# Kernel optimization log

Hardware: AMD Instinct MI355X
Metric: run time of the kernel (lower is better)

Reference implementation:

```python
import jax, jax.numpy as jnp
import numpy as np

LOSS_WEIGHT = 1.0
RADIUS = 1
DILATION = 2

def _mind_shift_indices():
    # six-neighbourhood offsets in a 3x3x3 kernel (as in torch code)
    six = np.array([[0, 1, 1], [1, 1, 0], [1, 0, 1], [1, 1, 2], [2, 1, 1], [1, 2, 1]])
    dist = ((six[:, None, :] - six[None, :, :]) ** 2).sum(-1)
    x, y = np.meshgrid(np.arange(6), np.arange(6), indexing='ij')
    mask = ((x > y) & (dist == 2)).reshape(-1)
    idx1 = np.repeat(six, 6, axis=0)[mask]
    idx2 = np.tile(six, (6, 1))[mask]
    return idx1, idx2

_IDX1, _IDX2 = _mind_shift_indices()

def _shifted(padded, idx, d, D, H, W):
    # one-hot dilated conv == static slice of replication-padded volume
    outs = [padded[:, :, a * d:a * d + D, b * d:b * d + H, c * d:c * d + W]
            for (a, b, c) in idx]
    return jnp.concatenate(outs, axis=1)  # (N, 12, D, H, W)

def mind_ssc(img, radius=RADIUS, dilation=DILATION):
    N, C, D, H, W = img.shape
    p = dilation
    padded = jnp.pad(img, ((0, 0), (0, 0), (p, p), (p, p), (p, p)), mode='edge')
    diff2 = (_shifted(padded, _IDX1, dilation, D, H, W)
             - _shifted(padded, _IDX2, dilation, D, H, W)) ** 2
    r = radius
    k = 2 * r + 1
    diff2p = jnp.pad(diff2, ((0, 0), (0, 0), (r, r), (r, r), (r, r)), mode='edge')
    ssd = jax.lax.reduce_window(diff2p, 0.0, jax.lax.add,
                                (1, 1, k, k, k), (1, 1, 1, 1, 1), 'VALID') / (k ** 3)
    mind = ssd - jnp.min(ssd, axis=1, keepdims=True)
    mind_var = jnp.mean(mind, axis=1, keepdims=True)
    m = jax.lax.stop_gradient(jnp.mean(mind_var))  # torch uses .item() -> detached
    mind_var = jnp.clip(mind_var, m * 0.001, m * 1000.0)
    return jnp.exp(-mind / mind_var)

def setup_inputs() -> dict:
    key = jax.random.key(0)
    k1, k2 = jax.random.split(key)
    shape = (2, 1, 128, 128, 128)
    predict = jax.random.normal(k1, shape, dtype=jnp.float32)
    target = jax.random.normal(k2, shape, dtype=jnp.float32)
    return {"predict": predict, "target": target}

def reference(predict, target):
    loss = jnp.mean((mind_ssc(predict) - mind_ssc(target)) ** 2)
    return loss * LOSS_WEIGHT
```

## Files before the change

### kernel.cpp

```cpp
#include <hip/hip_runtime.h>


#define DIM 128
#define HW (128 * 128)
#define DHW (128 * 128 * 128)
#define NVOX (2 * DHW)
#define LOSS_COUNT (2.0 * 12.0 * DHW)

#define TS   16
#define SY   18
#define NSP  (SY * TS)
#define CHZ  16
#define PSTR 7

typedef float f4 __attribute__((ext_vector_type(4)));
typedef float f2 __attribute__((ext_vector_type(2)));

__device__ __forceinline__ int clampi(int v) {
    v = v < 0 ? 0 : v;
    return v > 127 ? 127 : v;
}

__device__ __forceinline__ unsigned fkey(float f) {
    unsigned u = __float_as_uint(f);
    return (u & 0x80000000u) ? ~u : (u | 0x80000000u);
}
__device__ __forceinline__ float fdec(unsigned k) {
    unsigned u = (k & 0x80000000u) ? (k ^ 0x80000000u) : ~k;
    return __uint_as_float(u);
}

__device__ __forceinline__ void block_reduce_atomic(float v, double* dst) {
#pragma unroll
    for (int off = 32; off > 0; off >>= 1)
        v += __shfl_down(v, off, 64);
    __shared__ float red[4];
    int lane = threadIdx.x & 63;
    int wid  = threadIdx.x >> 6;
    if (lane == 0) red[wid] = v;
    __syncthreads();
    if (threadIdx.x == 0) {
        double t = (double)red[0] + (double)red[1] + (double)red[2] + (double)red[3];
        atomicAdd(dst, t);
    }
    __syncthreads();
}

__device__ __forceinline__ void block_minmax_atomic(float mnp, float mxp,
                                                    float mnt, float mxt,
                                                    unsigned* keys) {
#pragma unroll
    for (int off = 32; off > 0; off >>= 1) {
        mnp = fminf(mnp, __shfl_down(mnp, off, 64));
        mxp = fmaxf(mxp, __shfl_down(mxp, off, 64));
        mnt = fminf(mnt, __shfl_down(mnt, off, 64));
        mxt = fmaxf(mxt, __shfl_down(mxt, off, 64));
    }
    __shared__ float r[4][4];
    int lane = threadIdx.x & 63, wid = threadIdx.x >> 6;
    if (lane == 0) { r[wid][0] = mnp; r[wid][1] = mxp; r[wid][2] = mnt; r[wid][3] = mxt; }
    __syncthreads();
    if (threadIdx.x == 0) {
        float a = fminf(fminf(r[0][0], r[1][0]), fminf(r[2][0], r[3][0]));
        float b = fmaxf(fmaxf(r[0][1], r[1][1]), fmaxf(r[2][1], r[3][1]));
        float c = fminf(fminf(r[0][2], r[1][2]), fminf(r[2][2], r[3][2]));
        float d = fmaxf(fmaxf(r[0][3], r[1][3]), fmaxf(r[2][3], r[3][3]));
        atomicMin(&keys[0], fkey(a));
        atomicMax(&keys[1], fkey(b));
        atomicMin(&keys[2], fkey(c));
        atomicMax(&keys[3], fkey(d));
    }
    __syncthreads();
}

struct SPos {
    int y0, ym, yp;
    int cx[3], cm[3], cp[3];
    int woff;
};

__device__ __forceinline__ SPos make_spos(int p, int y0t, int x0t, int stride) {
    SPos q;
    int py = p >> 4, px = p & 15;
    int gy = clampi(y0t - 1 + py);
    int gx = x0t + px;
    q.y0 = gy * DIM; q.ym = clampi(gy - 2) * DIM; q.yp = clampi(gy + 2) * DIM;
#pragma unroll
    for (int wx = 0; wx < 3; ++wx) {
        int c = clampi(gx + wx - 1);
        q.cx[wx] = c;
        q.cm[wx] = clampi(c - 2);
        q.cp[wx] = clampi(c + 2);
    }
    q.woff = p * stride;
    return q;
}


__device__ __forceinline__ void stage_pair(const float* __restrict__ ip,
                                           const float* __restrict__ tp,
                                           int zm, int zc, int zp,
                                           const SPos& q, f4* __restrict__ X) {
    f2 acc[12];
#pragma unroll
    for (int c = 0; c < 12; ++c) acc[c] = (f2)0.0f;
#pragma unroll
    for (int wx = 0; wx < 3; ++wx) {
        int o0 = zm + q.y0 + q.cx[wx];
        int o1 = zc + q.y0 + q.cm[wx];
        int o2 = zc + q.ym + q.cx[wx];
        int o3 = zc + q.y0 + q.cp[wx];
        int o4 = zp + q.y0 + q.cx[wx];
        int o5 = zc + q.yp + q.cx[wx];
        f2 s0 = {ip[o0], tp[o0]};
        f2 s1 = {ip[o1], tp[o1]};
        f2 s2 = {ip[o2], tp[o2]};
        f2 s3 = {ip[o3], tp[o3]};
        f2 s4 = {ip[o4], tp[o4]};
        f2 s5 = {ip[o5], tp[o5]};
        f2 d;
        d = s1 - s0; acc[0]  += d * d;
        d = s2 - s0; acc[1]  += d * d;
        d = s2 - s1; acc[2]  += d * d;
        d = s3 - s0; acc[3]  += d * d;
        d = s3 - s2; acc[4]  += d * d;
        d = s4 - s1; acc[5]  += d * d;
        d = s4 - s2; acc[6]  += d * d;
        d = s4 - s3; acc[7]  += d * d;
        d = s5 - s0; acc[8]  += d * d;
        d = s5 - s1; acc[9]  += d * d;
        d = s5 - s3; acc[10] += d * d;
        d = s5 - s4; acc[11] += d * d;
    }
#pragma unroll
    for (int k = 0; k < 6; ++k) {
        f4 w;
        w.x = acc[2 * k].x;     w.y = acc[2 * k].y;
        w.z = acc[2 * k + 1].x; w.w = acc[2 * k + 1].y;
        X[q.woff + k] = w;
    }
}

__device__ __forceinline__ void box3y_pair(const f4* __restrict__ X,
                                           int ty, int tx, f4 q[6]) {
    int b0 = ((ty + 0) * TS + tx) * PSTR;
    int b1 = ((ty + 1) * TS + tx) * PSTR;
    int b2 = ((ty + 2) * TS + tx) * PSTR;
#pragma unroll
    for (int k = 0; k < 6; ++k)
        q[k] = X[b0 + k] + X[b1 + k] + X[b2 + k];
}

__global__ __launch_bounds__(256, 4) void fused_kernel(const float* __restrict__ pred,
                                                       const float* __restrict__ targ,
                                                       double* __restrict__ acc,
                                                       unsigned* __restrict__ keys) {
    __shared__ f4 X[NSP * PSTR];
    const int t = threadIdx.x;
    const int tile = blockIdx.x & 63, n = blockIdx.x >> 6;
    const int x0t = (tile & 7) * TS, y0t = (tile >> 3) * TS;
    const int z0 = blockIdx.y * CHZ;
    const float* ip = pred + (size_t)n * DHW;
    const float* tp = targ + (size_t)n * DHW;

    SPos pa = make_spos(t, y0t, x0t, PSTR);
    const bool hasB = (t + 256) < NSP;
    SPos pb = make_spos(hasB ? (t + 256) : 0, y0t, x0t, PSTR);

    const int ty = t >> 4, tx = t & 15;

    f4 A[6], B[6];
#pragma unroll
    for (int k = 0; k < 6; ++k) { A[k] = (f4)0.0f; B[k] = (f4)0.0f; }

    float vsump = 0.0f, vsumt = 0.0f, lsum = 0.0f;
    float locmnp = 1e30f, locmxp = -1e30f, locmnt = 1e30f, locmxt = -1e30f;

    for (int tz = z0 - 1; tz <= z0 + CHZ; ++tz) {
        int zq = clampi(tz);
        int zc = zq * HW, zm = clampi(zq - 2) * HW, zp = clampi(zq + 2) * HW;
        stage_pair(ip, tp, zm, zc, zp, pa, X);
        if (hasB) stage_pair(ip, tp, zm, zc, zp, pb, X);
        __syncthreads();

        f4 q[6];
        box3y_pair(X, ty, tx, q);
        __syncthreads();

        int ze = tz - 1;
        if (ze >= z0) {
            f4 v[6];
#pragma unroll
            for (int k = 0; k < 6; ++k) v[k] = A[k] + q[k];

            float mnp = v[0][0], mnt = v[0][1];
            float smp = 0.0f, smt = 0.0f;
#pragma unroll
            for (int c = 0; c < 12; ++c) {
                float pv = v[c >> 1][(c & 1) * 2];
                float tv = v[c >> 1][(c & 1) * 2 + 1];
                mnp = fminf(mnp, pv); smp += pv;
                mnt = fminf(mnt, tv); smt += tv;
            }
            float varp = smp * (1.0f / 12.0f) - mnp;
            float vart = smt * (1.0f / 12.0f) - mnt;
            vsump += varp; vsumt += vart;
            locmnp = fminf(locmnp, varp); locmxp = fmaxf(locmxp, varp);
            locmnt = fminf(locmnt, vart); locmxt = fmaxf(locmxt, vart);

            float invp = -1.0f / varp;
            float invt = -1.0f / vart;
            float la = 0.0f;
#pragma unroll
            for (int c = 0; c < 12; ++c) {
                float pv = v[c >> 1][(c & 1) * 2];
                float tv = v[c >> 1][(c & 1) * 2 + 1];
                float ep = __expf((pv - mnp) * invp);
                float et = __expf((tv - mnt) * invt);
                float dd = ep - et;
                la += dd * dd;
            }
            lsum += la;
        }
#pragma unroll
        for (int k = 0; k < 6; ++k) { A[k] = B[k] + q[k]; B[k] = q[k]; }
    }

    block_reduce_atomic(vsump, &acc[0]);
    block_reduce_atomic(vsumt, &acc[1]);
    block_reduce_atomic(lsum,  &acc[2]);
    block_minmax_atomic(locmnp, locmxp, locmnt, locmxt, keys);
}


__global__ void init_kernel(double* __restrict__ acc, unsigned* __restrict__ keys) {
    acc[0] = 0.0; acc[1] = 0.0; acc[2] = 0.0; acc[3] = 0.0;
    keys[0] = 0xFFFFFFFFu; keys[1] = 0u;
    keys[2] = 0xFFFFFFFFu; keys[3] = 0u;
    keys[4] = 0u;
}

__global__ void flag_kernel(const double* __restrict__ acc, unsigned* __restrict__ keys) {
    float m_p = (float)(acc[0] * (1.0 / (double)NVOX));
    float m_t = (float)(acc[1] * (1.0 / (double)NVOX));
    float mnp = fdec(keys[0]), mxp = fdec(keys[1]);
    float mnt = fdec(keys[2]), mxt = fdec(keys[3]);
    bool clean = (mnp >= m_p * 0.001f) && (mxp <= m_p * 1000.0f) &&
                 (mnt >= m_t * 0.001f) && (mxt <= m_t * 1000.0f);
    keys[4] = clean ? 0u : 1u;
}

__device__ __forceinline__ void stage_xsum(const float* __restrict__ im,
                                           int zm, int zc, int zp,
                                           const SPos& q, f4* __restrict__ P) {
    f4 a = (f4)0.0f, b = (f4)0.0f, c = (f4)0.0f;
#pragma unroll
    for (int wx = 0; wx < 3; ++wx) {
        float s0 = im[zm + q.y0 + q.cx[wx]];
        float s1 = im[zc + q.y0 + q.cm[wx]];
        float s2 = im[zc + q.ym + q.cx[wx]];
        float s3 = im[zc + q.y0 + q.cp[wx]];
        float s4 = im[zp + q.y0 + q.cx[wx]];
        float s5 = im[zc + q.yp + q.cx[wx]];
        float d;
        d = s1 - s0; a.x += d * d;
        d = s2 - s0; a.y += d * d;
        d = s2 - s1; a.z += d * d;
        d = s3 - s0; a.w += d * d;
        d = s3 - s2; b.x += d * d;
        d = s4 - s1; b.y += d * d;
        d = s4 - s2; b.z += d * d;
        d = s4 - s3; b.w += d * d;
        d = s5 - s0; c.x += d * d;
        d = s5 - s1; c.y += d * d;
        d = s5 - s3; c.z += d * d;
        d = s5 - s4; c.w += d * d;
    }
    P[q.woff + 0] = a;
    P[q.woff + 1] = b;
    P[q.woff + 2] = c;
}

__device__ __forceinline__ void box3y(const f4* __restrict__ P,
                                      int ty, int tx, f4 q[3]) {
    int base = (ty * TS + tx) * 3;
#pragma unroll
    for (int k = 0; k < 3; ++k)
        q[k] = P[base + k] + P[base + TS * 3 + k] + P[base + 2 * TS * 3 + k];
}

__device__ __forceinline__ float min12(const f4 v[3]) {
    float mn = v[0][0];
#pragma unroll
    for (int i = 0; i < 4; ++i)
        mn = fminf(mn, fminf(v[0][i], fminf(v[1][i], v[2][i])));
    return mn;
}
__device__ __forceinline__ float sum12(const f4 v[3]) {
    float sm = 0.0f;
#pragma unroll
    for (int i = 0; i < 4; ++i)
        sm += v[0][i] + v[1][i] + v[2][i];
    return sm;
}

__global__ __launch_bounds__(256, 4) void loss_kernel(const float* __restrict__ pred,
                                                      const float* __restrict__ targ,
                                                      const double* __restrict__ acc,
                                                      const unsigned* __restrict__ keys,
                                                      double* __restrict__ loss_sum) {
    if (keys[4] == 0u) return;

    __shared__ f4 Xp[NSP * 3];
    __shared__ f4 Xt[NSP * 3];
    const int t = threadIdx.x;
    const int tile = blockIdx.x & 63, n = blockIdx.x >> 6;
    const int x0t = (tile & 7) * TS, y0t = (tile >> 3) * TS;
    const int z0 = blockIdx.y * CHZ;
    const float* ip = pred + (size_t)n * DHW;
    const float* tp = targ + (size_t)n * DHW;

    const float m_p = (float)(acc[0] * (1.0 / (double)NVOX));
    const float m_t = (float)(acc[1] * (1.0 / (double)NVOX));

    SPos pa = make_spos(t, y0t, x0t, 3);
    const bool hasB = (t + 256) < NSP;
    SPos pb = make_spos(hasB ? (t + 256) : 0, y0t, x0t, 3);

    const int ty = t >> 4, tx = t & 15;

    f4 Ap[3], Bp[3], At[3], Bt[3];
#pragma unroll
    for (int q = 0; q < 3; ++q) {
        Ap[q] = (f4)0.0f; Bp[q] = (f4)0.0f;
        At[q] = (f4)0.0f; Bt[q] = (f4)0.0f;
    }
    float lsum = 0.0f;

    for (int tz = z0 - 1; tz <= z0 + CHZ; ++tz) {
        int zq = clampi(tz);
        int zc = zq * HW, zm = clampi(zq - 2) * HW, zp = clampi(zq + 2) * HW;
        stage_xsum(ip, zm, zc, zp, pa, Xp);
        stage_xsum(tp, zm, zc, zp, pa, Xt);
        if (hasB) {
            stage_xsum(ip, zm, zc, zp, pb, Xp);
            stage_xsum(tp, zm, zc, zp, pb, Xt);
        }
        __syncthreads();

        f4 qp[3], qt[3];
        box3y(Xp, ty, tx, qp);
        box3y(Xt, ty, tx, qt);
        __syncthreads();

        int ze = tz - 1;
        if (ze >= z0) {
            f4 vp[3], vt[3];
#pragma unroll
            for (int q = 0; q < 3; ++q) {
                vp[q] = Ap[q] + qp[q];
                vt[q] = At[q] + qt[q];
            }
            float mnp = min12(vp), smp = sum12(vp);
            float mnt = min12(vt), smt = sum12(vt);
            float varp = smp * (1.0f / 12.0f) - mnp;
            varp = fminf(fmaxf(varp, m_p * 0.001f), m_p * 1000.0f);
            float invp = -1.0f / varp;
            float vart = smt * (1.0f / 12.0f) - mnt;
            vart = fminf(fmaxf(vart, m_t * 0.001f), m_t * 1000.0f);
            float invt = -1.0f / vart;

            float a = 0.0f;
#pragma unroll
            for (int q = 0; q < 3; ++q)
#pragma unroll
                for (int i = 0; i < 4; ++i) {
                    float ep = __expf((vp[q][i] - mnp) * invp);
                    float et = __expf((vt[q][i] - mnt) * invt);
                    float dd = ep - et;
                    a += dd * dd;
                }
            lsum += a;
        }
#pragma unroll
        for (int q = 0; q < 3; ++q) {
            Ap[q] = Bp[q] + qp[q]; Bp[q] = qp[q];
            At[q] = Bt[q] + qt[q]; Bt[q] = qt[q];
        }
    }

    block_reduce_atomic(lsum, loss_sum);
}

__global__ void finalize_kernel(const double* __restrict__ acc,
                                const unsigned* __restrict__ keys,
                                float* __restrict__ out) {
    double l = (keys[4] == 0u) ? acc[2] : acc[3];
    out[0] = (float)(l * (1.0 / LOSS_COUNT));
}

extern "C" void kernel_launch(void* const* d_in, const int* in_sizes, int n_in,
                              void* d_out, int out_size, void* d_ws, size_t ws_size,
                              hipStream_t stream) {
    const float* pred = (const float*)d_in[0];
    const float* targ = (const float*)d_in[1];
    float* out = (float*)d_out;
    double* acc = (double*)d_ws;
    unsigned* keys = (unsigned*)((char*)d_ws + 64);

    dim3 block(256);
    dim3 grid(128, 8);

    init_kernel<<<1, 1, 0, stream>>>(acc, keys);
    fused_kernel<<<grid, block, 0, stream>>>(pred, targ, acc, keys);
    flag_kernel<<<1, 1, 0, stream>>>(acc, keys);
    loss_kernel<<<grid, block, 0, stream>>>(pred, targ, acc, keys, &acc[3]);
    finalize_kernel<<<1, 1, 0, stream>>>(acc, keys, out);
}
```

Measured before the change: 167.0 us.

## Merge five launches into one cooperative kernel with grid syncs

Result: slower. 519.2 us (+210.9%).

```diff
diff --git a/kernel.cpp b/kernel.cpp
--- a/kernel.cpp
+++ b/kernel.cpp
@@ -1,5 +1,8 @@
 #include <hip/hip_runtime.h>
-
+#include <hip/hip_cooperative_groups.h>
+
+
+namespace cg = cooperative_groups;
 
 #define DIM 128
 #define HW (128 * 128)
@@ -96,22 +99,23 @@
     return q;
 }
 
-
 __device__ __forceinline__ void stage_pair(const float* __restrict__ ip,
                                            const float* __restrict__ tp,
                                            int zm, int zc, int zp,
                                            const SPos& q, f4* __restrict__ X) {
+    const int r0 = zm + q.y0, r1 = zc + q.y0, r2 = zc + q.ym;
+    const int r3 = zc + q.yp, r4 = zp + q.y0;
     f2 acc[12];
 #pragma unroll
     for (int c = 0; c < 12; ++c) acc[c] = (f2)0.0f;
 #pragma unroll
     for (int wx = 0; wx < 3; ++wx) {
-        int o0 = zm + q.y0 + q.cx[wx];
-        int o1 = zc + q.y0 + q.cm[wx];
-        int o2 = zc + q.ym + q.cx[wx];
-        int o3 = zc + q.y0 + q.cp[wx];
-        int o4 = zp + q.y0 + q.cx[wx];
-        int o5 = zc + q.yp + q.cx[wx];
+        int o0 = r0 + q.cx[wx];
+        int o1 = r1 + q.cm[wx];
+        int o2 = r2 + q.cx[wx];
+        int o3 = r1 + q.cp[wx];
+        int o4 = r4 + q.cx[wx];
+        int o5 = r3 + q.cx[wx];
         f2 s0 = {ip[o0], tp[o0]};
         f2 s1 = {ip[o1], tp[o1]};
         f2 s2 = {ip[o2], tp[o2]};
@@ -151,117 +155,20 @@
         q[k] = X[b0 + k] + X[b1 + k] + X[b2 + k];
 }
 
-__global__ __launch_bounds__(256, 4) void fused_kernel(const float* __restrict__ pred,
-                                                       const float* __restrict__ targ,
-                                                       double* __restrict__ acc,
-                                                       unsigned* __restrict__ keys) {
-    __shared__ f4 X[NSP * PSTR];
-    const int t = threadIdx.x;
-    const int tile = blockIdx.x & 63, n = blockIdx.x >> 6;
-    const int x0t = (tile & 7) * TS, y0t = (tile >> 3) * TS;
-    const int z0 = blockIdx.y * CHZ;
-    const float* ip = pred + (size_t)n * DHW;
-    const float* tp = targ + (size_t)n * DHW;
-
-    SPos pa = make_spos(t, y0t, x0t, PSTR);
-    const bool hasB = (t + 256) < NSP;
-    SPos pb = make_spos(hasB ? (t + 256) : 0, y0t, x0t, PSTR);
-
-    const int ty = t >> 4, tx = t & 15;
-
-    f4 A[6], B[6];
-#pragma unroll
-    for (int k = 0; k < 6; ++k) { A[k] = (f4)0.0f; B[k] = (f4)0.0f; }
-
-    float vsump = 0.0f, vsumt = 0.0f, lsum = 0.0f;
-    float locmnp = 1e30f, locmxp = -1e30f, locmnt = 1e30f, locmxt = -1e30f;
-
-    for (int tz = z0 - 1; tz <= z0 + CHZ; ++tz) {
-        int zq = clampi(tz);
-        int zc = zq * HW, zm = clampi(zq - 2) * HW, zp = clampi(zq + 2) * HW;
-        stage_pair(ip, tp, zm, zc, zp, pa, X);
-        if (hasB) stage_pair(ip, tp, zm, zc, zp, pb, X);
-        __syncthreads();
-
-        f4 q[6];
-        box3y_pair(X, ty, tx, q);
-        __syncthreads();
-
-        int ze = tz - 1;
-        if (ze >= z0) {
-            f4 v[6];
-#pragma unroll
-            for (int k = 0; k < 6; ++k) v[k] = A[k] + q[k];
-
-            float mnp = v[0][0], mnt = v[0][1];
-            float smp = 0.0f, smt = 0.0f;
-#pragma unroll
-            for (int c = 0; c < 12; ++c) {
-                float pv = v[c >> 1][(c & 1) * 2];
-                float tv = v[c >> 1][(c & 1) * 2 + 1];
-                mnp = fminf(mnp, pv); smp += pv;
-                mnt = fminf(mnt, tv); smt += tv;
-            }
-            float varp = smp * (1.0f / 12.0f) - mnp;
-            float vart = smt * (1.0f / 12.0f) - mnt;
-            vsump += varp; vsumt += vart;
-            locmnp = fminf(locmnp, varp); locmxp = fmaxf(locmxp, varp);
-            locmnt = fminf(locmnt, vart); locmxt = fmaxf(locmxt, vart);
-
-            float invp = -1.0f / varp;
-            float invt = -1.0f / vart;
-            float la = 0.0f;
-#pragma unroll
-            for (int c = 0; c < 12; ++c) {
-                float pv = v[c >> 1][(c & 1) * 2];
-                float tv = v[c >> 1][(c & 1) * 2 + 1];
-                float ep = __expf((pv - mnp) * invp);
-                float et = __expf((tv - mnt) * invt);
-                float dd = ep - et;
-                la += dd * dd;
-            }
-            lsum += la;
-        }
-#pragma unroll
-        for (int k = 0; k < 6; ++k) { A[k] = B[k] + q[k]; B[k] = q[k]; }
-    }
-
-    block_reduce_atomic(vsump, &acc[0]);
-    block_reduce_atomic(vsumt, &acc[1]);
-    block_reduce_atomic(lsum,  &acc[2]);
-    block_minmax_atomic(locmnp, locmxp, locmnt, locmxt, keys);
-}
-
-
-__global__ void init_kernel(double* __restrict__ acc, unsigned* __restrict__ keys) {
-    acc[0] = 0.0; acc[1] = 0.0; acc[2] = 0.0; acc[3] = 0.0;
-    keys[0] = 0xFFFFFFFFu; keys[1] = 0u;
-    keys[2] = 0xFFFFFFFFu; keys[3] = 0u;
-    keys[4] = 0u;
-}
-
-__global__ void flag_kernel(const double* __restrict__ acc, unsigned* __restrict__ keys) {
-    float m_p = (float)(acc[0] * (1.0 / (double)NVOX));
-    float m_t = (float)(acc[1] * (1.0 / (double)NVOX));
-    float mnp = fdec(keys[0]), mxp = fdec(keys[1]);
-    float mnt = fdec(keys[2]), mxt = fdec(keys[3]);
-    bool clean = (mnp >= m_p * 0.001f) && (mxp <= m_p * 1000.0f) &&
-                 (mnt >= m_t * 0.001f) && (mxt <= m_t * 1000.0f);
-    keys[4] = clean ? 0u : 1u;
-}
-
 __device__ __forceinline__ void stage_xsum(const float* __restrict__ im,
                                            int zm, int zc, int zp,
                                            const SPos& q, f4* __restrict__ P) {
+    const int r0 = zm + q.y0, r1 = zc + q.y0, r2 = zc + q.ym;
+    const int r3 = zc + q.yp, r4 = zp + q.y0;
     f4 a = (f4)0.0f, b = (f4)0.0f, c = (f4)0.0f;
 #pragma unroll
     for (int wx = 0; wx < 3; ++wx) {
-        float s0 = im[zm + q.y0 + q.cx[wx]];
-        float s1 = im[zc + q.y0 + q.cm[wx]];
-        float s2 = im[zc + q.ym + q.cx[wx]];
-        float s3 = im[zc + q.y0 + q.cp[wx]];
-        float s4 = im[zp + q.y0 + q.cx[wx]];
-        float s5 = im[zc + q.yp + q.cx[wx]];
+        float s0 = im[r0 + q.cx[wx]];
+        float s1 = im[r1 + q.cm[wx]];
+        float s2 = im[r2 + q.cx[wx]];
+        float s3 = im[r1 + q.cp[wx]];
+        float s4 = im[r4 + q.cx[wx]];
+        float s5 = im[r3 + q.cx[wx]];
         float d;
         d = s1 - s0; a.x += d * d;
         d = s2 - s0; a.y += d * d;
@@ -304,6 +211,293 @@
     return sm;
 }
 
+
+__global__ __launch_bounds__(256, 4) void mono_kernel(const float* __restrict__ pred,
+                                                      const float* __restrict__ targ,
+                                                      double* __restrict__ acc,
+                                                      unsigned* __restrict__ keys,
+                                                      float* __restrict__ out) {
+    cg::grid_group grid = cg::this_grid();
+
+    __shared__ f4 X[NSP * PSTR];
+
+    const int t = threadIdx.x;
+    const int tile = blockIdx.x & 63, n = blockIdx.x >> 6;
+    const int x0t = (tile & 7) * TS, y0t = (tile >> 3) * TS;
+    const int z0 = blockIdx.y * CHZ;
+    const float* ip = pred + (size_t)n * DHW;
+    const float* tp = targ + (size_t)n * DHW;
+    const bool isB0 = (blockIdx.x == 0 && blockIdx.y == 0);
+
+    if (isB0 && t == 0) {
+        acc[0] = 0.0; acc[1] = 0.0; acc[2] = 0.0; acc[3] = 0.0;
+        keys[0] = 0xFFFFFFFFu; keys[1] = 0u;
+        keys[2] = 0xFFFFFFFFu; keys[3] = 0u;
+    }
+    grid.sync();
+
+    SPos pa = make_spos(t, y0t, x0t, PSTR);
+    const bool hasB = (t + 256) < NSP;
+    SPos pb = make_spos(hasB ? (t + 256) : 0, y0t, x0t, PSTR);
+    const int ty = t >> 4, tx = t & 15;
+
+    {
+        f4 A[6], B[6];
+#pragma unroll
+        for (int k = 0; k < 6; ++k) { A[k] = (f4)0.0f; B[k] = (f4)0.0f; }
+
+        float vsump = 0.0f, vsumt = 0.0f, lsum = 0.0f;
+        float locmnp = 1e30f, locmxp = -1e30f, locmnt = 1e30f, locmxt = -1e30f;
+
+        for (int tz = z0 - 1; tz <= z0 + CHZ; ++tz) {
+            int zq = clampi(tz);
+            int zc = zq * HW, zm = clampi(zq - 2) * HW, zp = clampi(zq + 2) * HW;
+            stage_pair(ip, tp, zm, zc, zp, pa, X);
+            if (hasB) stage_pair(ip, tp, zm, zc, zp, pb, X);
+            __syncthreads();
+
+            f4 q[6];
+            box3y_pair(X, ty, tx, q);
+            __syncthreads();
+
+            int ze = tz - 1;
+            if (ze >= z0) {
+                f4 v[6];
+#pragma unroll
+                for (int k = 0; k < 6; ++k) v[k] = A[k] + q[k];
+
+                float mnp = v[0][0], mnt = v[0][1];
+                float smp = 0.0f, smt = 0.0f;
+#pragma unroll
+                for (int c = 0; c < 12; ++c) {
+                    float pv = v[c >> 1][(c & 1) * 2];
+                    float tv = v[c >> 1][(c & 1) * 2 + 1];
+                    mnp = fminf(mnp, pv); smp += pv;
+                    mnt = fminf(mnt, tv); smt += tv;
+                }
+                float varp = smp * (1.0f / 12.0f) - mnp;
+                float vart = smt * (1.0f / 12.0f) - mnt;
+                vsump += varp; vsumt += vart;
+                locmnp = fminf(locmnp, varp); locmxp = fmaxf(locmxp, varp);
+                locmnt = fminf(locmnt, vart); locmxt = fmaxf(locmxt, vart);
+
+                float invp = -1.0f / varp;
+                float invt = -1.0f / vart;
+                float la = 0.0f;
+#pragma unroll
+                for (int c = 0; c < 12; ++c) {
+                    float pv = v[c >> 1][(c & 1) * 2];
+                    float tv = v[c >> 1][(c & 1) * 2 + 1];
+                    float ep = __expf((pv - mnp) * invp);
+                    float et = __expf((tv - mnt) * invt);
+                    float dd = ep - et;
+                    la += dd * dd;
+                }
+                lsum += la;
+            }
+#pragma unroll
+            for (int k = 0; k < 6; ++k) { A[k] = B[k] + q[k]; B[k] = q[k]; }
+        }
+
+        block_reduce_atomic(vsump, &acc[0]);
+        block_reduce_atomic(vsumt, &acc[1]);
+        block_reduce_atomic(lsum,  &acc[2]);
+        block_minmax_atomic(locmnp, locmxp, locmnt, locmxt, keys);
+    }
+    __threadfence();
+    grid.sync();
+
+    __shared__ float s_mp, s_mt;
+    __shared__ int s_clean;
+    if (t == 0) {
+        double a0 = __hip_atomic_load(&acc[0], __ATOMIC_RELAXED, __HIP_MEMORY_SCOPE_AGENT);
+        double a1 = __hip_atomic_load(&acc[1], __ATOMIC_RELAXED, __HIP_MEMORY_SCOPE_AGENT);
+        unsigned k0 = __hip_atomic_load(&keys[0], __ATOMIC_RELAXED, __HIP_MEMORY_SCOPE_AGENT);
+        unsigned k1 = __hip_atomic_load(&keys[1], __ATOMIC_RELAXED, __HIP_MEMORY_SCOPE_AGENT);
+        unsigned k2 = __hip_atomic_load(&keys[2], __ATOMIC_RELAXED, __HIP_MEMORY_SCOPE_AGENT);
+        unsigned k3 = __hip_atomic_load(&keys[3], __ATOMIC_RELAXED, __HIP_MEMORY_SCOPE_AGENT);
+        float m_p = (float)(a0 * (1.0 / (double)NVOX));
+        float m_t = (float)(a1 * (1.0 / (double)NVOX));
+        bool clean = (fdec(k0) >= m_p * 0.001f) && (fdec(k1) <= m_p * 1000.0f) &&
+                     (fdec(k2) >= m_t * 0.001f) && (fdec(k3) <= m_t * 1000.0f);
+        s_mp = m_p; s_mt = m_t; s_clean = clean ? 1 : 0;
+    }
+    __syncthreads();
+    const bool clean = (s_clean != 0);
+    const float m_p = s_mp, m_t = s_mt;
+
+    if (!clean) {
+        f4* Xp = X;
+        f4* Xt = X + NSP * 3;
+        SPos fa = make_spos(t, y0t, x0t, 3);
+        SPos fb = make_spos(hasB ? (t + 256) : 0, y0t, x0t, 3);
+
+        f4 Ap[3], Bp[3], At[3], Bt[3];
+#pragma unroll
+        for (int q = 0; q < 3; ++q) {
+            Ap[q] = (f4)0.0f; Bp[q] = (f4)0.0f;
+            At[q] = (f4)0.0f; Bt[q] = (f4)0.0f;
+        }
+        float lsum = 0.0f;
+
+        for (int tz = z0 - 1; tz <= z0 + CHZ; ++tz) {
+            int zq = clampi(tz);
+            int zc = zq * HW, zm = clampi(zq - 2) * HW, zp = clampi(zq + 2) * HW;
+            stage_xsum(ip, zm, zc, zp, fa, Xp);
+            stage_xsum(tp, zm, zc, zp, fa, Xt);
+            if (hasB) {
+                stage_xsum(ip, zm, zc, zp, fb, Xp);
+                stage_xsum(tp, zm, zc, zp, fb, Xt);
+            }
+            __syncthreads();
+
+            f4 qp[3], qt[3];
+            box3y(Xp, ty, tx, qp);
+            box3y(Xt, ty, tx, qt);
+            __syncthreads();
+
+            int ze = tz - 1;
+            if (ze >= z0) {
+                f4 vp[3], vt[3];
+#pragma unroll
+                for (int q = 0; q < 3; ++q) {
+                    vp[q] = Ap[q] + qp[q];
+                    vt[q] = At[q] + qt[q];
+                }
+                float mnp = min12(vp), smp = sum12(vp);
+                float mnt = min12(vt), smt = sum12(vt);
+                float varp = smp * (1.0f / 12.0f) - mnp;
+                varp = fminf(fmaxf(varp, m_p * 0.001f), m_p * 1000.0f);
+                float invp = -1.0f / varp;
+                float vart = smt * (1.0f / 12.0f) - mnt;
+                vart = fminf(fmaxf(vart, m_t * 0.001f), m_t * 1000.0f);
+                float invt = -1.0f / vart;
+
+                float a = 0.0f;
+#pragma unroll
+                for (int q = 0; q < 3; ++q)
+#pragma unroll
+                    for (int i = 0; i < 4; ++i) {
+                        float ep = __expf((vp[q][i] - mnp) * invp);
+                        float et = __expf((vt[q][i] - mnt) * invt);
+                        float dd = ep - et;
+                        a += dd * dd;
+                    }
+                lsum += a;
+            }
+#pragma unroll
+            for (int q = 0; q < 3; ++q) {
+                Ap[q] = Bp[q] + qp[q]; Bp[q] = qp[q];
+                At[q] = Bt[q] + qt[q]; Bt[q] = qt[q];
+            }
+        }
+        block_reduce_atomic(lsum, &acc[3]);
+        __threadfence();
+    }
+    grid.sync();
+
+    if (isB0 && t == 0) {
+        double l = clean
+            ? __hip_atomic_load(&acc[2], __ATOMIC_RELAXED, __HIP_MEMORY_SCOPE_AGENT)
+            : __hip_atomic_load(&acc[3], __ATOMIC_RELAXED, __HIP_MEMORY_SCOPE_AGENT);
+        out[0] = (float)(l * (1.0 / LOSS_COUNT));
+    }
+}
+
+
+__global__ void init_kernel(double* __restrict__ acc, unsigned* __restrict__ keys) {
+    acc[0] = 0.0; acc[1] = 0.0; acc[2] = 0.0; acc[3] = 0.0;
+    keys[0] = 0xFFFFFFFFu; keys[1] = 0u;
+    keys[2] = 0xFFFFFFFFu; keys[3] = 0u;
+    keys[4] = 0u;
+}
+
+__global__ __launch_bounds__(256, 4) void fused_kernel(const float* __restrict__ pred,
+                                                       const float* __restrict__ targ,
+                                                       double* __restrict__ acc,
+                                                       unsigned* __restrict__ keys) {
+    __shared__ f4 X[NSP * PSTR];
+    const int t = threadIdx.x;
+    const int tile = blockIdx.x & 63, n = blockIdx.x >> 6;
+    const int x0t = (tile & 7) * TS, y0t = (tile >> 3) * TS;
+    const int z0 = blockIdx.y * CHZ;
+    const float* ip = pred + (size_t)n * DHW;
+    const float* tp = targ + (size_t)n * DHW;
+
+    SPos pa = make_spos(t, y0t, x0t, PSTR);
+    const bool hasB = (t + 256) < NSP;
+    SPos pb = make_spos(hasB ? (t + 256) : 0, y0t, x0t, PSTR);
+    const int ty = t >> 4, tx = t & 15;
+
+    f4 A[6], B[6];
+#pragma unroll
+    for (int k = 0; k < 6; ++k) { A[k] = (f4)0.0f; B[k] = (f4)0.0f; }
+
+    float vsump = 0.0f, vsumt = 0.0f, lsum = 0.0f;
+    float locmnp = 1e30f, locmxp = -1e30f, locmnt = 1e30f, locmxt = -1e30f;
+
+    for (int tz = z0 - 1; tz <= z0 + CHZ; ++tz) {
+        int zq = clampi(tz);
+        int zc = zq * HW, zm = clampi(zq - 2) * HW, zp = clampi(zq + 2) * HW;
+        stage_pair(ip, tp, zm, zc, zp, pa, X);
+        if (hasB) stage_pair(ip, tp, zm, zc, zp, pb, X);
+        __syncthreads();
+
+        f4 q[6];
+        box3y_pair(X, ty, tx, q);
+        __syncthreads();
+
+        int ze = tz - 1;
+        if (ze >= z0) {
+            f4 v[6];
+#pragma unroll
+            for (int k = 0; k < 6; ++k) v[k] = A[k] + q[k];
+            float mnp = v[0][0], mnt = v[0][1];
+            float smp = 0.0f, smt = 0.0f;
+#pragma unroll
+            for (int c = 0; c < 12; ++c) {
+                float pv = v[c >> 1][(c & 1) * 2];
+                float tv = v[c >> 1][(c & 1) * 2 + 1];
+                mnp = fminf(mnp, pv); smp += pv;
+                mnt = fminf(mnt, tv); smt += tv;
+            }
+            float varp = smp * (1.0f / 12.0f) - mnp;
+            float vart = smt * (1.0f / 12.0f) - mnt;
+            vsump += varp; vsumt += vart;
+            locmnp = fminf(locmnp, varp); locmxp = fmaxf(locmxp, varp);
+            locmnt = fminf(locmnt, vart); locmxt = fmaxf(locmxt, vart);
+            float invp = -1.0f / varp;
+            float invt = -1.0f / vart;
+            float la = 0.0f;
+#pragma unroll
+            for (int c = 0; c < 12; ++c) {
+                float pv = v[c >> 1][(c & 1) * 2];
+                float tv = v[c >> 1][(c & 1) * 2 + 1];
+                float ep = __expf((pv - mnp) * invp);
+                float et = __expf((tv - mnt) * invt);
+                float dd = ep - et;
+                la += dd * dd;
+            }
+            lsum += la;
+        }
+#pragma unroll
+        for (int k = 0; k < 6; ++k) { A[k] = B[k] + q[k]; B[k] = q[k]; }
+    }
+
+    block_reduce_atomic(vsump, &acc[0]);
+    block_reduce_atomic(vsumt, &acc[1]);
+    block_reduce_atomic(lsum,  &acc[2]);
+    block_minmax_atomic(locmnp, locmxp, locmnt, locmxt, keys);
+}
+
+__global__ void flag_kernel(const double* __restrict__ acc, unsigned* __restrict__ keys) {
+    float m_p = (float)(acc[0] * (1.0 / (double)NVOX));
+    float m_t = (float)(acc[1] * (1.0 / (double)NVOX));
+    bool clean = (fdec(keys[0]) >= m_p * 0.001f) && (fdec(keys[1]) <= m_p * 1000.0f) &&
+                 (fdec(keys[2]) >= m_t * 0.001f) && (fdec(keys[3]) <= m_t * 1000.0f);
+    keys[4] = clean ? 0u : 1u;
+}
+
 __global__ __launch_bounds__(256, 4) void loss_kernel(const float* __restrict__ pred,
                                                       const float* __restrict__ targ,
                                                       const double* __restrict__ acc,
@@ -326,7 +520,6 @@
     SPos pa = make_spos(t, y0t, x0t, 3);
     const bool hasB = (t + 256) < NSP;
     SPos pb = make_spos(hasB ? (t + 256) : 0, y0t, x0t, 3);
-
     const int ty = t >> 4, tx = t & 15;
 
     f4 Ap[3], Bp[3], At[3], Bt[3];
@@ -411,9 +604,14 @@
     dim3 block(256);
     dim3 grid(128, 8);
 
-    init_kernel<<<1, 1, 0, stream>>>(acc, keys);
-    fused_kernel<<<grid, block, 0, stream>>>(pred, targ, acc, keys);
-    flag_kernel<<<1, 1, 0, stream>>>(acc, keys);
-    loss_kernel<<<grid, block, 0, stream>>>(pred, targ, acc, keys, &acc[3]);
-    finalize_kernel<<<1, 1, 0, stream>>>(acc, keys, out);
-}
+    void* args[] = {(void*)&pred, (void*)&targ, (void*)&acc, (void*)&keys, (void*)&out};
+    hipError_t e = hipLaunchCooperativeKernel((void*)mono_kernel, grid, block,
+                                              args, 0, stream);
+    if (e != hipSuccess) {
+        init_kernel<<<1, 1, 0, stream>>>(acc, keys);
+        fused_kernel<<<grid, block, 0, stream>>>(pred, targ, acc, keys);
+        flag_kernel<<<1, 1, 0, stream>>>(acc, keys);
+        loss_kernel<<<grid, block, 0, stream>>>(pred, targ, acc, keys, &acc[3]);
+        finalize_kernel<<<1, 1, 0, stream>>>(acc, keys, out);
+    }
+}
```

## Fold init/flag/finalize kernels into last-block reductions with per-block partials

Applied to the files above, without the earlier changes.

New measurement: 197.8 us. +18.4%, slower.

```diff
diff --git a/kernel.cpp b/kernel.cpp
--- a/kernel.cpp
+++ b/kernel.cpp
@@ -12,65 +12,29 @@
 #define NSP  (SY * TS)
 #define CHZ  16
 #define PSTR 7
+#define NBLK 1024
 
 typedef float f4 __attribute__((ext_vector_type(4)));
 typedef float f2 __attribute__((ext_vector_type(2)));
+
+struct Header {
+    unsigned counter0;
+    unsigned counter1;
+    unsigned flag;
+    float m_p, m_t;
+    unsigned pad;
+    double acc_clip;
+};
+
+struct Partial {
+    double vsump, vsumt, lsum;
+    float mnp, mxp, mnt, mxt;
+    float pad[6];
+};
 
 __device__ __forceinline__ int clampi(int v) {
     v = v < 0 ? 0 : v;
     return v > 127 ? 127 : v;
-}
-
-__device__ __forceinline__ unsigned fkey(float f) {
-    unsigned u = __float_as_uint(f);
-    return (u & 0x80000000u) ? ~u : (u | 0x80000000u);
-}
-__device__ __forceinline__ float fdec(unsigned k) {
-    unsigned u = (k & 0x80000000u) ? (k ^ 0x80000000u) : ~k;
-    return __uint_as_float(u);
-}
-
-__device__ __forceinline__ void block_reduce_atomic(float v, double* dst) {
-#pragma unroll
-    for (int off = 32; off > 0; off >>= 1)
-        v += __shfl_down(v, off, 64);
-    __shared__ float red[4];
-    int lane = threadIdx.x & 63;
-    int wid  = threadIdx.x >> 6;
-    if (lane == 0) red[wid] = v;
-    __syncthreads();
-    if (threadIdx.x == 0) {
-        double t = (double)red[0] + (double)red[1] + (double)red[2] + (double)red[3];
-        atomicAdd(dst, t);
-    }
-    __syncthreads();
-}
-
-__device__ __forceinline__ void block_minmax_atomic(float mnp, float mxp,
-                                                    float mnt, float mxt,
-                                                    unsigned* keys) {
-#pragma unroll
-    for (int off = 32; off > 0; off >>= 1) {
-        mnp = fminf(mnp, __shfl_down(mnp, off, 64));
-        mxp = fmaxf(mxp, __shfl_down(mxp, off, 64));
-        mnt = fminf(mnt, __shfl_down(mnt, off, 64));
-        mxt = fmaxf(mxt, __shfl_down(mxt, off, 64));
-    }
-    __shared__ float r[4][4];
-    int lane = threadIdx.x & 63, wid = threadIdx.x >> 6;
-    if (lane == 0) { r[wid][0] = mnp; r[wid][1] = mxp; r[wid][2] = mnt; r[wid][3] = mxt; }
-    __syncthreads();
-    if (threadIdx.x == 0) {
-        float a = fminf(fminf(r[0][0], r[1][0]), fminf(r[2][0], r[3][0]));
-        float b = fmaxf(fmaxf(r[0][1], r[1][1]), fmaxf(r[2][1], r[3][1]));
-        float c = fminf(fminf(r[0][2], r[1][2]), fminf(r[2][2], r[3][2]));
-        float d = fmaxf(fmaxf(r[0][3], r[1][3]), fmaxf(r[2][3], r[3][3]));
-        atomicMin(&keys[0], fkey(a));
-        atomicMax(&keys[1], fkey(b));
-        atomicMin(&keys[2], fkey(c));
-        atomicMax(&keys[3], fkey(d));
-    }
-    __syncthreads();
 }
 
 struct SPos {
@@ -96,22 +60,23 @@
     return q;
 }
 
-
 __device__ __forceinline__ void stage_pair(const float* __restrict__ ip,
                                            const float* __restrict__ tp,
                                            int zm, int zc, int zp,
                                            const SPos& q, f4* __restrict__ X) {
+    const int r0 = zm + q.y0, r1 = zc + q.y0, r2 = zc + q.ym;
+    const int r3 = zc + q.yp, r4 = zp + q.y0;
     f2 acc[12];
 #pragma unroll
     for (int c = 0; c < 12; ++c) acc[c] = (f2)0.0f;
 #pragma unroll
     for (int wx = 0; wx < 3; ++wx) {
-        int o0 = zm + q.y0 + q.cx[wx];
-        int o1 = zc + q.y0 + q.cm[wx];
-        int o2 = zc + q.ym + q.cx[wx];
-        int o3 = zc + q.y0 + q.cp[wx];
-        int o4 = zp + q.y0 + q.cx[wx];
-        int o5 = zc + q.yp + q.cx[wx];
+        int o0 = r0 + q.cx[wx];
+        int o1 = r1 + q.cm[wx];
+        int o2 = r2 + q.cx[wx];
+        int o3 = r1 + q.cp[wx];
+        int o4 = r4 + q.cx[wx];
+        int o5 = r3 + q.cx[wx];
         f2 s0 = {ip[o0], tp[o0]};
         f2 s1 = {ip[o1], tp[o1]};
         f2 s2 = {ip[o2], tp[o2]};
@@ -151,117 +116,20 @@
         q[k] = X[b0 + k] + X[b1 + k] + X[b2 + k];
 }
 
-__global__ __launch_bounds__(256, 4) void fused_kernel(const float* __restrict__ pred,
-                                                       const float* __restrict__ targ,
-                                                       double* __restrict__ acc,
-                                                       unsigned* __restrict__ keys) {
-    __shared__ f4 X[NSP * PSTR];
-    const int t = threadIdx.x;
-    const int tile = blockIdx.x & 63, n = blockIdx.x >> 6;
-    const int x0t = (tile & 7) * TS, y0t = (tile >> 3) * TS;
-    const int z0 = blockIdx.y * CHZ;
-    const float* ip = pred + (size_t)n * DHW;
-    const float* tp = targ + (size_t)n * DHW;
-
-    SPos pa = make_spos(t, y0t, x0t, PSTR);
-    const bool hasB = (t + 256) < NSP;
-    SPos pb = make_spos(hasB ? (t + 256) : 0, y0t, x0t, PSTR);
-
-    const int ty = t >> 4, tx = t & 15;
-
-    f4 A[6], B[6];
-#pragma unroll
-    for (int k = 0; k < 6; ++k) { A[k] = (f4)0.0f; B[k] = (f4)0.0f; }
-
-    float vsump = 0.0f, vsumt = 0.0f, lsum = 0.0f;
-    float locmnp = 1e30f, locmxp = -1e30f, locmnt = 1e30f, locmxt = -1e30f;
-
-    for (int tz = z0 - 1; tz <= z0 + CHZ; ++tz) {
-        int zq = clampi(tz);
-        int zc = zq * HW, zm = clampi(zq - 2) * HW, zp = clampi(zq + 2) * HW;
-        stage_pair(ip, tp, zm, zc, zp, pa, X);
-        if (hasB) stage_pair(ip, tp, zm, zc, zp, pb, X);
-        __syncthreads();
-
-        f4 q[6];
-        box3y_pair(X, ty, tx, q);
-        __syncthreads();
-
-        int ze = tz - 1;
-        if (ze >= z0) {
-            f4 v[6];
-#pragma unroll
-            for (int k = 0; k < 6; ++k) v[k] = A[k] + q[k];
-
-            float mnp = v[0][0], mnt = v[0][1];
-            float smp = 0.0f, smt = 0.0f;
-#pragma unroll
-            for (int c = 0; c < 12; ++c) {
-                float pv = v[c >> 1][(c & 1) * 2];
-                float tv = v[c >> 1][(c & 1) * 2 + 1];
-                mnp = fminf(mnp, pv); smp += pv;
-                mnt = fminf(mnt, tv); smt += tv;
-            }
-            float varp = smp * (1.0f / 12.0f) - mnp;
-            float vart = smt * (1.0f / 12.0f) - mnt;
-            vsump += varp; vsumt += vart;
-            locmnp = fminf(locmnp, varp); locmxp = fmaxf(locmxp, varp);
-            locmnt = fminf(locmnt, vart); locmxt = fmaxf(locmxt, vart);
-
-            float invp = -1.0f / varp;
-            float invt = -1.0f / vart;
-            float la = 0.0f;
-#pragma unroll
-            for (int c = 0; c < 12; ++c) {
-                float pv = v[c >> 1][(c & 1) * 2];
-                float tv = v[c >> 1][(c & 1) * 2 + 1];
-                float ep = __expf((pv - mnp) * invp);
-                float et = __expf((tv - mnt) * invt);
-                float dd = ep - et;
-                la += dd * dd;
-            }
-            lsum += la;
-        }
-#pragma unroll
-        for (int k = 0; k < 6; ++k) { A[k] = B[k] + q[k]; B[k] = q[k]; }
-    }
-
-    block_reduce_atomic(vsump, &acc[0]);
-    block_reduce_atomic(vsumt, &acc[1]);
-    block_reduce_atomic(lsum,  &acc[2]);
-    block_minmax_atomic(locmnp, locmxp, locmnt, locmxt, keys);
-}
-
-
-__global__ void init_kernel(double* __restrict__ acc, unsigned* __restrict__ keys) {
-    acc[0] = 0.0; acc[1] = 0.0; acc[2] = 0.0; acc[3] = 0.0;
-    keys[0] = 0xFFFFFFFFu; keys[1] = 0u;
-    keys[2] = 0xFFFFFFFFu; keys[3] = 0u;
-    keys[4] = 0u;
-}
-
-__global__ void flag_kernel(const double* __restrict__ acc, unsigned* __restrict__ keys) {
-    float m_p = (float)(acc[0] * (1.0 / (double)NVOX));
-    float m_t = (float)(acc[1] * (1.0 / (double)NVOX));
-    float mnp = fdec(keys[0]), mxp = fdec(keys[1]);
-    float mnt = fdec(keys[2]), mxt = fdec(keys[3]);
-    bool clean = (mnp >= m_p * 0.001f) && (mxp <= m_p * 1000.0f) &&
-                 (mnt >= m_t * 0.001f) && (mxt <= m_t * 1000.0f);
-    keys[4] = clean ? 0u : 1u;
-}
-
 __device__ __forceinline__ void stage_xsum(const float* __restrict__ im,
                                            int zm, int zc, int zp,
                                            const SPos& q, f4* __restrict__ P) {
+    const int r0 = zm + q.y0, r1 = zc + q.y0, r2 = zc + q.ym;
+    const int r3 = zc + q.yp, r4 = zp + q.y0;
     f4 a = (f4)0.0f, b = (f4)0.0f, c = (f4)0.0f;
 #pragma unroll
     for (int wx = 0; wx < 3; ++wx) {
-        float s0 = im[zm + q.y0 + q.cx[wx]];
-        float s1 = im[zc + q.y0 + q.cm[wx]];
-        float s2 = im[zc + q.ym + q.cx[wx]];
-        float s3 = im[zc + q.y0 + q.cp[wx]];
-        float s4 = im[zp + q.y0 + q.cx[wx]];
-        float s5 = im[zc + q.yp + q.cx[wx]];
+        float s0 = im[r0 + q.cx[wx]];
+        float s1 = im[r1 + q.cm[wx]];
+        float s2 = im[r2 + q.cx[wx]];
+        float s3 = im[r1 + q.cp[wx]];
+        float s4 = im[r4 + q.cx[wx]];
+        float s5 = im[r3 + q.cx[wx]];
         float d;
         d = s1 - s0; a.x += d * d;
         d = s2 - s0; a.y += d * d;
@@ -304,12 +172,187 @@
     return sm;
 }
 
+
+__global__ __launch_bounds__(256, 4) void fused_kernel(const float* __restrict__ pred,
+                                                       const float* __restrict__ targ,
+                                                       Header* __restrict__ hdr,
+                                                       Partial* __restrict__ parts,
+                                                       float* __restrict__ out) {
+    __shared__ f4 X[NSP * PSTR];
+
+    const int t = threadIdx.x;
+    const int tile = blockIdx.x & 63, n = blockIdx.x >> 6;
+    const int x0t = (tile & 7) * TS, y0t = (tile >> 3) * TS;
+    const int z0 = blockIdx.y * CHZ;
+    const int bid = blockIdx.y * gridDim.x + blockIdx.x;
+    const float* ip = pred + (size_t)n * DHW;
+    const float* tp = targ + (size_t)n * DHW;
+
+    SPos pa = make_spos(t, y0t, x0t, PSTR);
+    const bool hasB = (t + 256) < NSP;
+    SPos pb = make_spos(hasB ? (t + 256) : 0, y0t, x0t, PSTR);
+    const int ty = t >> 4, tx = t & 15;
+
+    f4 A[6], B[6];
+#pragma unroll
+    for (int k = 0; k < 6; ++k) { A[k] = (f4)0.0f; B[k] = (f4)0.0f; }
+
+    float vsump = 0.0f, vsumt = 0.0f, lsum = 0.0f;
+    float locmnp = 1e30f, locmxp = -1e30f, locmnt = 1e30f, locmxt = -1e30f;
+
+    for (int tz = z0 - 1; tz <= z0 + CHZ; ++tz) {
+        int zq = clampi(tz);
+        int zc = zq * HW, zm = clampi(zq - 2) * HW, zp = clampi(zq + 2) * HW;
+        stage_pair(ip, tp, zm, zc, zp, pa, X);
+        if (hasB) stage_pair(ip, tp, zm, zc, zp, pb, X);
+        __syncthreads();
+
+        f4 q[6];
+        box3y_pair(X, ty, tx, q);
+        __syncthreads();
+
+        int ze = tz - 1;
+        if (ze >= z0) {
+            f4 v[6];
+#pragma unroll
+            for (int k = 0; k < 6; ++k) v[k] = A[k] + q[k];
+
+            float mnp = v[0][0], mnt = v[0][1];
+            float smp = 0.0f, smt = 0.0f;
+#pragma unroll
+            for (int c = 0; c < 12; ++c) {
+                float pv = v[c >> 1][(c & 1) * 2];
+                float tv = v[c >> 1][(c & 1) * 2 + 1];
+                mnp = fminf(mnp, pv); smp += pv;
+                mnt = fminf(mnt, tv); smt += tv;
+            }
+            float varp = smp * (1.0f / 12.0f) - mnp;
+            float vart = smt * (1.0f / 12.0f) - mnt;
+            vsump += varp; vsumt += vart;
+            locmnp = fminf(locmnp, varp); locmxp = fmaxf(locmxp, varp);
+            locmnt = fminf(locmnt, vart); locmxt = fmaxf(locmxt, vart);
+
+            float invp = -1.0f / varp;
+            float invt = -1.0f / vart;
+            float la = 0.0f;
+#pragma unroll
+            for (int c = 0; c < 12; ++c) {
+                float pv = v[c >> 1][(c & 1) * 2];
+                float tv = v[c >> 1][(c & 1) * 2 + 1];
+                float ep = __expf((pv - mnp) * invp);
+                float et = __expf((tv - mnt) * invt);
+                float dd = ep - et;
+                la += dd * dd;
+            }
+            lsum += la;
+        }
+#pragma unroll
+        for (int k = 0; k < 6; ++k) { A[k] = B[k] + q[k]; B[k] = q[k]; }
+    }
+
+#pragma unroll
+    for (int off = 32; off > 0; off >>= 1) {
+        vsump += __shfl_down(vsump, off, 64);
+        vsumt += __shfl_down(vsumt, off, 64);
+        lsum  += __shfl_down(lsum,  off, 64);
+        locmnp = fminf(locmnp, __shfl_down(locmnp, off, 64));
+        locmxp = fmaxf(locmxp, __shfl_down(locmxp, off, 64));
+        locmnt = fminf(locmnt, __shfl_down(locmnt, off, 64));
+        locmxt = fmaxf(locmxt, __shfl_down(locmxt, off, 64));
+    }
+    __shared__ float rs[4][7];
+    __shared__ int s_tail;
+    {
+        int lane = t & 63, wid = t >> 6;
+        if (lane == 0) {
+            rs[wid][0] = vsump; rs[wid][1] = vsumt; rs[wid][2] = lsum;
+            rs[wid][3] = locmnp; rs[wid][4] = locmxp;
+            rs[wid][5] = locmnt; rs[wid][6] = locmxt;
+        }
+    }
+    __syncthreads();
+    if (t == 0) {
+        double d0 = (double)rs[0][0] + rs[1][0] + rs[2][0] + rs[3][0];
+        double d1 = (double)rs[0][1] + rs[1][1] + rs[2][1] + rs[3][1];
+        double d2 = (double)rs[0][2] + rs[1][2] + rs[2][2] + rs[3][2];
+        float a = fminf(fminf(rs[0][3], rs[1][3]), fminf(rs[2][3], rs[3][3]));
+        float b = fmaxf(fmaxf(rs[0][4], rs[1][4]), fmaxf(rs[2][4], rs[3][4]));
+        float c = fminf(fminf(rs[0][5], rs[1][5]), fminf(rs[2][5], rs[3][5]));
+        float d = fmaxf(fmaxf(rs[0][6], rs[1][6]), fmaxf(rs[2][6], rs[3][6]));
+        Partial* p = &parts[bid];
+        __hip_atomic_store(&p->vsump, d0, __ATOMIC_RELAXED, __HIP_MEMORY_SCOPE_AGENT);
+        __hip_atomic_store(&p->vsumt, d1, __ATOMIC_RELAXED, __HIP_MEMORY_SCOPE_AGENT);
+        __hip_atomic_store(&p->lsum,  d2, __ATOMIC_RELAXED, __HIP_MEMORY_SCOPE_AGENT);
+        __hip_atomic_store(&p->mnp, a, __ATOMIC_RELAXED, __HIP_MEMORY_SCOPE_AGENT);
+        __hip_atomic_store(&p->mxp, b, __ATOMIC_RELAXED, __HIP_MEMORY_SCOPE_AGENT);
+        __hip_atomic_store(&p->mnt, c, __ATOMIC_RELAXED, __HIP_MEMORY_SCOPE_AGENT);
+        __hip_atomic_store(&p->mxt, d, __ATOMIC_RELAXED, __HIP_MEMORY_SCOPE_AGENT);
+        unsigned old = __hip_atomic_fetch_add(&hdr->counter0, 1u,
+                                              __ATOMIC_ACQ_REL, __HIP_MEMORY_SCOPE_AGENT);
+        s_tail = (old == NBLK - 1) ? 1 : 0;
+    }
+    __syncthreads();
+
+    if (s_tail) {
+        double vp = 0.0, vt = 0.0, ls = 0.0;
+        float mnp = 1e30f, mxp = -1e30f, mnt = 1e30f, mxt = -1e30f;
+        for (int b = t; b < NBLK; b += 256) {
+            const Partial* p = &parts[b];
+            vp += __hip_atomic_load(&p->vsump, __ATOMIC_RELAXED, __HIP_MEMORY_SCOPE_AGENT);
+            vt += __hip_atomic_load(&p->vsumt, __ATOMIC_RELAXED, __HIP_MEMORY_SCOPE_AGENT);
+            ls += __hip_atomic_load(&p->lsum,  __ATOMIC_RELAXED, __HIP_MEMORY_SCOPE_AGENT);
+            mnp = fminf(mnp, __hip_atomic_load(&p->mnp, __ATOMIC_RELAXED, __HIP_MEMORY_SCOPE_AGENT));
+            mxp = fmaxf(mxp, __hip_atomic_load(&p->mxp, __ATOMIC_RELAXED, __HIP_MEMORY_SCOPE_AGENT));
+            mnt = fminf(mnt, __hip_atomic_load(&p->mnt, __ATOMIC_RELAXED, __HIP_MEMORY_SCOPE_AGENT));
+            mxt = fmaxf(mxt, __hip_atomic_load(&p->mxt, __ATOMIC_RELAXED, __HIP_MEMORY_SCOPE_AGENT));
+        }
+#pragma unroll
+        for (int off = 32; off > 0; off >>= 1) {
+            vp += __shfl_down(vp, off, 64);
+            vt += __shfl_down(vt, off, 64);
+            ls += __shfl_down(ls, off, 64);
+            mnp = fminf(mnp, __shfl_down(mnp, off, 64));
+            mxp = fmaxf(mxp, __shfl_down(mxp, off, 64));
+            mnt = fminf(mnt, __shfl_down(mnt, off, 64));
+            mxt = fmaxf(mxt, __shfl_down(mxt, off, 64));
+        }
+        __shared__ double rd[4][3];
+        __shared__ float rf[4][4];
+        int lane = t & 63, wid = t >> 6;
+        if (lane == 0) {
+            rd[wid][0] = vp; rd[wid][1] = vt; rd[wid][2] = ls;
+            rf[wid][0] = mnp; rf[wid][1] = mxp; rf[wid][2] = mnt; rf[wid][3] = mxt;
+        }
+        __syncthreads();
+        if (t == 0) {
+            double VP = rd[0][0] + rd[1][0] + rd[2][0] + rd[3][0];
+            double VT = rd[0][1] + rd[1][1] + rd[2][1] + rd[3][1];
+            double LS = rd[0][2] + rd[1][2] + rd[2][2] + rd[3][2];
+            float MNP = fminf(fminf(rf[0][0], rf[1][0]), fminf(rf[2][0], rf[3][0]));
+            float MXP = fmaxf(fmaxf(rf[0][1], rf[1][1]), fmaxf(rf[2][1], rf[3][1]));
+            float MNT = fminf(fminf(rf[0][2], rf[1][2]), fminf(rf[2][2], rf[3][2]));
+            float MXT = fmaxf(fmaxf(rf[0][3], rf[1][3]), fmaxf(rf[2][3], rf[3][3]));
+            float m_p = (float)(VP * (1.0 / (double)NVOX));
+            float m_t = (float)(VT * (1.0 / (double)NVOX));
+            bool clean = (MNP >= m_p * 0.001f) && (MXP <= m_p * 1000.0f) &&
+                         (MNT >= m_t * 0.001f) && (MXT <= m_t * 1000.0f);
+            hdr->m_p = m_p;
+            hdr->m_t = m_t;
+            __hip_atomic_store(&hdr->acc_clip, 0.0, __ATOMIC_RELAXED, __HIP_MEMORY_SCOPE_AGENT);
+            __hip_atomic_store(&hdr->flag, clean ? 0u : 1u,
+                               __ATOMIC_RELEASE, __HIP_MEMORY_SCOPE_AGENT);
+            if (clean) out[0] = (float)(LS * (1.0 / LOSS_COUNT));
+        }
+    }
+}
+
+
 __global__ __launch_bounds__(256, 4) void loss_kernel(const float* __restrict__ pred,
                                                       const float* __restrict__ targ,
-                                                      const double* __restrict__ acc,
-                                                      const unsigned* __restrict__ keys,
-                                                      double* __restrict__ loss_sum) {
-    if (keys[4] == 0u) return;
+                                                      Header* __restrict__ hdr,
+                                                      float* __restrict__ out) {
+    if (__hip_atomic_load(&hdr->flag, __ATOMIC_ACQUIRE, __HIP_MEMORY_SCOPE_AGENT) == 0u)
+        return;
 
     __shared__ f4 Xp[NSP * 3];
     __shared__ f4 Xt[NSP * 3];
@@ -320,13 +363,12 @@
     const float* ip = pred + (size_t)n * DHW;
     const float* tp = targ + (size_t)n * DHW;
 
-    const float m_p = (float)(acc[0] * (1.0 / (double)NVOX));
-    const float m_t = (float)(acc[1] * (1.0 / (double)NVOX));
+    const float m_p = hdr->m_p;
+    const float m_t = hdr->m_t;
 
     SPos pa = make_spos(t, y0t, x0t, 3);
     const bool hasB = (t + 256) < NSP;
     SPos pb = make_spos(hasB ? (t + 256) : 0, y0t, x0t, 3);
-
     const int ty = t >> 4, tx = t & 15;
 
     f4 Ap[3], Bp[3], At[3], Bt[3];
@@ -389,14 +431,24 @@
         }
     }
 
-    block_reduce_atomic(lsum, loss_sum);
-}
-
-__global__ void finalize_kernel(const double* __restrict__ acc,
-                                const unsigned* __restrict__ keys,
-                                float* __restrict__ out) {
-    double l = (keys[4] == 0u) ? acc[2] : acc[3];
-    out[0] = (float)(l * (1.0 / LOSS_COUNT));
+#pragma unroll
+    for (int off = 32; off > 0; off >>= 1)
+        lsum += __shfl_down(lsum, off, 64);
+    __shared__ float red[4];
+    int lane = t & 63, wid = t >> 6;
+    if (lane == 0) red[wid] = lsum;
+    __syncthreads();
+    if (t == 0) {
+        double tt = (double)red[0] + red[1] + red[2] + red[3];
+        atomicAdd(&hdr->acc_clip, tt);
+        unsigned old = __hip_atomic_fetch_add(&hdr->counter1, 1u,
+                                              __ATOMIC_ACQ_REL, __HIP_MEMORY_SCOPE_AGENT);
+        if (old == NBLK - 1) {
+            double l = __hip_atomic_load(&hdr->acc_clip, __ATOMIC_RELAXED,
+                                         __HIP_MEMORY_SCOPE_AGENT);
+            out[0] = (float)(l * (1.0 / LOSS_COUNT));
+        }
+    }
 }
 
 extern "C" void kernel_launch(void* const* d_in, const int* in_sizes, int n_in,
@@ -405,15 +457,13 @@
     const float* pred = (const float*)d_in[0];
     const float* targ = (const float*)d_in[1];
     float* out = (float*)d_out;
-    double* acc = (double*)d_ws;
-    unsigned* keys = (unsigned*)((char*)d_ws + 64);
+    Header* hdr = (Header*)d_ws;
+    Partial* parts = (Partial*)((char*)d_ws + 256);
+
+    hipMemsetAsync(d_ws, 0, 256, stream);
 
     dim3 block(256);
     dim3 grid(128, 8);
-
-    init_kernel<<<1, 1, 0, stream>>>(acc, keys);
-    fused_kernel<<<grid, block, 0, stream>>>(pred, targ, acc, keys);
-    flag_kernel<<<1, 1, 0, stream>>>(acc, keys);
-    loss_kernel<<<grid, block, 0, stream>>>(pred, targ, acc, keys, &acc[3]);
-    finalize_kernel<<<1, 1, 0, stream>>>(acc, keys, out);
-}
+    fused_kernel<<<grid, block, 0, stream>>>(pred, targ, hdr, parts, out);
+    loss_kernel<<<grid, block, 0, stream>>>(pred, targ, hdr, out);
+}
```
